# Performance work log

Hardware: AMD Instinct MI355X
Metric: run time of the kernel (lower is better)

Reference implementation:

```python
import jax, jax.numpy as jnp
import numpy as np

DIM = 768
N_HEADS = 12
HEAD_DIM = DIM // N_HEADS
SCALE = HEAD_DIM ** (-0.5)


def setup_inputs() -> dict:
    key = jax.random.key(0)
    k1, k2, k3 = jax.random.split(key, 3)
    B, S = 8, 1024
    x = jax.random.normal(k1, (B, S, DIM), dtype=jnp.float32)
    qkv_w = jax.random.normal(k2, (3 * DIM, DIM), dtype=jnp.float32) * (DIM ** -0.5)
    qkv_b = jnp.zeros((3 * DIM,), dtype=jnp.float32)
    proj_w = jax.random.normal(k3, (DIM, DIM), dtype=jnp.float32) * (DIM ** -0.5)
    proj_b = jnp.zeros((DIM,), dtype=jnp.float32)
    return {"x": x, "qkv_w": qkv_w, "qkv_b": qkv_b, "proj_w": proj_w, "proj_b": proj_b}


def reference(x, qkv_w, qkv_b, proj_w, proj_b):
    B, S, D = x.shape
    # qkv projection: (B,S,3D)
    qkv = jnp.einsum('bsd,ed->bse', x, qkv_w) + qkv_b
    qkv = qkv.reshape(B, S, 3, N_HEADS, HEAD_DIM)
    q, k, v = qkv[:, :, 0], qkv[:, :, 1], qkv[:, :, 2]  # each (B,S,H,Dh)
    # scaled dot-product attention, materializing (B,H,S,S) as the original does
    scores = jnp.einsum('bqhd,bkhd->bhqk', q, k) * SCALE
    attn = jax.nn.softmax(scores, axis=-1)
    out = jnp.einsum('bhqk,bkhd->bqhd', attn, v).reshape(B, S, D)
    # output projection
    return jnp.einsum('bsd,ed->bse', out, proj_w) + proj_b
```

## Files before the change

### kernel.cpp

```cpp
#include <hip/hip_runtime.h>
#include <hip/hip_bf16.h>


typedef __attribute__((ext_vector_type(4))) float  f32x4;
typedef __attribute__((ext_vector_type(8))) short  short8;
typedef __attribute__((ext_vector_type(4))) short  short4v;
typedef __attribute__((ext_vector_type(2))) unsigned int uint2v;

__device__ __forceinline__ unsigned short f2bf_hw(float f) {
  return __builtin_bit_cast(unsigned short, __float2bfloat16(f));
}
__device__ __forceinline__ unsigned int pk2bf(float a, float b) {
  return (unsigned int)f2bf_hw(a) | ((unsigned int)f2bf_hw(b) << 16);
}

#define MFMA16(a, b, c) __builtin_amdgcn_mfma_f32_16x16x32_bf16((a), (b), (c), 0, 0, 0)

#define QSCALE 0.18033688011112042f

__device__ __forceinline__ void gload_lds16(const unsigned short* g, char* lds) {
  __builtin_amdgcn_global_load_lds(
      (const __attribute__((address_space(1))) unsigned int*)g,
      (__attribute__((address_space(3))) unsigned int*)lds, 16, 0, 0);
}

__global__ __launch_bounds__(256)
void cvt3(const float* __restrict__ a, unsigned short* __restrict__ da, int na,
          const float* __restrict__ b, unsigned short* __restrict__ db, int nb,
          const float* __restrict__ c, unsigned short* __restrict__ dc)
{
  int i = blockIdx.x * 256 + threadIdx.x;
  const float* s; unsigned short* d;
  if (i < na)           { s = a; d = da; }
  else if (i < na + nb) { s = b; d = db; i -= na; }
  else                  { s = c; d = dc; i -= na + nb; }
  f32x4 v = ((const f32x4*)s)[i];
  short4v h;
  h[0] = (short)f2bf_hw(v[0]); h[1] = (short)f2bf_hw(v[1]);
  h[2] = (short)f2bf_hw(v[2]); h[3] = (short)f2bf_hw(v[3]);
  ((short4v*)d)[i] = h;
}

template<int EPI>
__global__ __launch_bounds__(256)
void gemm_bt(const unsigned short* __restrict__ A, const unsigned short* __restrict__ Wb,
             const float* __restrict__ bias,
             unsigned short* __restrict__ Qt, unsigned short* __restrict__ Kt,
             unsigned short* __restrict__ Vt, float* __restrict__ Out)
{
  __shared__ char lds[65536];
  const int tid = threadIdx.x;
  const int w = tid >> 6, l = tid & 63, lr = l & 15, lg = l >> 4;
  const int wr = w >> 1, wc = w & 1;
  const int m0 = blockIdx.x * 128, n0 = blockIdx.y * 128;
  f32x4 acc[4][4] = {};

  const int srow = tid >> 3;
  const int cb   = ((tid & 7) << 4) ^ ((srow & 7) << 4);
  const unsigned short* pA = A  + (size_t)(m0 + srow) * 768 + (cb >> 1);
  const unsigned short* pW = Wb + (size_t)(n0 + srow) * 768 + (cb >> 1);
  char* const ldsA = lds + tid * 16;
  char* const ldsW = lds + 16384 + tid * 16;

  #pragma unroll
  for (int c = 0; c < 4; ++c) gload_lds16(pA + c * 32 * 768, ldsA + c * 4096);
  #pragma unroll
  for (int c = 0; c < 4; ++c) gload_lds16(pW + c * 32 * 768, ldsW + c * 4096);
  pA += 64; pW += 64;

  for (int kt = 0; kt < 12; ++kt) {
    if (kt < 11) {
      const int nb = ((kt + 1) & 1) * 32768;
      #pragma unroll
      for (int c = 0; c < 4; ++c) gload_lds16(pA + c * 32 * 768, ldsA + nb + c * 4096);
      #pragma unroll
      for (int c = 0; c < 4; ++c) gload_lds16(pW + c * 32 * 768, ldsW + nb + c * 4096);
      pA += 64; pW += 64;
      asm volatile("s_waitcnt vmcnt(8)" ::: "memory");
    } else {
      asm volatile("s_waitcnt vmcnt(0)" ::: "memory");
    }
    __builtin_amdgcn_s_barrier();
    __builtin_amdgcn_sched_barrier(0);

    const char* Ab = lds + (kt & 1) * 32768;
    const char* Bb = Ab + 16384;
    #pragma unroll
    for (int kc = 0; kc < 2; ++kc) {
      short8 af[4], bfr[4];
      #pragma unroll
      for (int mf = 0; mf < 4; ++mf) {
        const int row = wr * 64 + mf * 16 + lr;
        af[mf] = *(const short8*)(Ab + row * 128 +
                                  ((kc * 64 + lg * 16) ^ ((row & 7) << 4)));
      }
      #pragma unroll
      for (int nf = 0; nf < 4; ++nf) {
        const int row = wc * 64 + nf * 16 + lr;
        bfr[nf] = *(const short8*)(Bb + row * 128 +
                                   ((kc * 64 + lg * 16) ^ ((row & 7) << 4)));
      }
      #pragma unroll
      for (int mf = 0; mf < 4; ++mf)
        #pragma unroll
        for (int nf = 0; nf < 4; ++nf)
          acc[mf][nf] = MFMA16(af[mf], bfr[nf], acc[mf][nf]);
    }
    __builtin_amdgcn_s_barrier();
  }

  if constexpr (EPI == 0) {
    const int tt = blockIdx.y / 6;
    const int h = (blockIdx.y % 6) * 2 + wc;
    #pragma unroll
    for (int nf = 0; nf < 4; ++nf) {
      const int dh = nf * 16 + lr;
      const float bv = bias[n0 + wc * 64 + dh];
      #pragma unroll
      for (int mf = 0; mf < 4; ++mf) {
        const int mb = m0 + wr * 64 + mf * 16 + lg * 4;
        const int b_ = mb >> 10, s_ = mb & 1023;
        f32x4 c = acc[mf][nf];
        if (tt == 0) {
          unsigned short* p = Qt + ((b_ * 12 + h) * 1024 + s_) * 64 + dh;
          #pragma unroll
          for (int j = 0; j < 4; ++j) p[j * 64] = f2bf_hw((c[j] + bv) * QSCALE);
        } else if (tt == 1) {
          unsigned short* p = Kt + ((b_ * 12 + h) * 1024 + s_) * 64 + dh;
          #pragma unroll
          for (int j = 0; j < 4; ++j) p[j * 64] = f2bf_hw(c[j] + bv);
        } else {
          short4v pk;
          #pragma unroll
          for (int j = 0; j < 4; ++j) pk[j] = (short)f2bf_hw(c[j] + bv);
          *(short4v*)(Vt + ((b_ * 12 + h) * 64 + dh) * 1024 + s_) = pk;
        }
      }
    }
  } else {
    #pragma unroll
    for (int nf = 0; nf < 4; ++nf) {
      const int e = n0 + wc * 64 + nf * 16 + lr;
      const float bv = bias[e];
      #pragma unroll
      for (int mf = 0; mf < 4; ++mf) {
        const int mb = m0 + wr * 64 + mf * 16 + lg * 4;
        #pragma unroll
        for (int j = 0; j < 4; ++j)
          Out[(size_t)(mb + j) * 768 + e] = acc[mf][nf][j] + bv;
      }
    }
  }
}

__global__ __launch_bounds__(256, 4)
void attn_fwd(const unsigned short* __restrict__ Qt,
              const unsigned short* __restrict__ Kt,
              const unsigned short* __restrict__ Vt,
              unsigned short* __restrict__ AO)
{
  __shared__ char lds[40960];
  char* Ks = lds;
  char* Vs = lds + 16384;
  char* Ps = lds + 32768;

  const int bid = blockIdx.x;
  const int bh = bid % 96, qt = bid / 96;
  const int tid = threadIdx.x, w = tid >> 6, l = tid & 63, lr = l & 15, lg = l >> 4;
  const unsigned short* Qh = Qt + bh * 65536;
  const unsigned short* Kh = Kt + bh * 65536;
  const unsigned short* Vh = Vt + bh * 65536;
  const int b_ = bh / 12, h = bh % 12;

  const int srow = tid >> 3;
  const int cb   = ((tid & 7) << 4) ^ ((srow & 7) << 4);
  char* const ldsK = Ks + tid * 16;
  char* const ldsV = Vs + tid * 16;
  char* const Pw = Ps + w * 2048;
  const int pswz = (lr & 7) << 4;

  #pragma unroll
  for (int c = 0; c < 2; ++c)
    gload_lds16(Kh + (size_t)(srow + c * 32) * 64 + (cb >> 1), ldsK + c * 4096);
  #pragma unroll
  for (int c = 0; c < 2; ++c)
    gload_lds16(Vh + (size_t)(srow + c * 32) * 1024 + (cb >> 1), ldsV + c * 4096);
  __syncthreads();

  for (int qs = 0; qs < 2; ++qs) {
    const int q0 = qt * 128 + qs * 64 + w * 16;
    const short8 aq0 = *(const short8*)(Qh + (q0 + lr) * 64 + lg * 8);
    const short8 aq1 = *(const short8*)(Qh + (q0 + lr) * 64 + 32 + lg * 8);

    float mr = -1e30f, lsum = 0.f;
    f32x4 o[4] = {};

    for (int t = 0; t < 16; ++t) {
      const int cur = t & 1;
      if (!(qs == 1 && t == 15)) {
        const int nk = ((t + 1) & 15) * 64;
        const int nb = (cur ^ 1) * 8192;
        #pragma unroll
        for (int c = 0; c < 2; ++c)
          gload_lds16(Kh + (size_t)(nk + srow + c * 32) * 64 + (cb >> 1),
                      ldsK + nb + c * 4096);
        #pragma unroll
        for (int c = 0; c < 2; ++c)
          gload_lds16(Vh + (size_t)(srow + c * 32) * 1024 + nk + (cb >> 1),
                      ldsV + nb + c * 4096);
      }

      const char* Kb = Ks + cur * 8192;
      f32x4 sf[4];
      __builtin_amdgcn_s_setprio(1);
      #pragma unroll
      for (int kf = 0; kf < 4; ++kf) {
        const char* base = Kb + (kf * 16 + lr) * 128;
        short8 b0 = *(const short8*)(base + ((lg * 16) ^ pswz));
        short8 b1 = *(const short8*)(base + ((64 + lg * 16) ^ pswz));
        f32x4 c = {};
        c = MFMA16(b0, aq0, c);
        c = MFMA16(b1, aq1, c);
        sf[kf] = c;
      }
      __builtin_amdgcn_s_setprio(0);

      float tm = fmaxf(fmaxf(sf[0][0], sf[0][1]), fmaxf(sf[0][2], sf[0][3]));
      #pragma unroll
      for (int kf = 1; kf < 4; ++kf)
        tm = fmaxf(tm, fmaxf(fmaxf(sf[kf][0], sf[kf][1]), fmaxf(sf[kf][2], sf[kf][3])));
      tm = fmaxf(tm, __shfl_xor(tm, 16));
      tm = fmaxf(tm, __shfl_xor(tm, 32));

      if (__any(tm > mr + 8.0f)) {
        const float mn = fmaxf(mr, tm);
        const float corr = exp2f(mr - mn);
        lsum *= corr;
        #pragma unroll
        for (int cf = 0; cf < 4; ++cf)
          #pragma unroll
          for (int j = 0; j < 4; ++j) o[cf][j] *= corr;
        mr = mn;
      }

      float ts = 0.f;
      #pragma unroll
      for (int kf = 0; kf < 4; ++kf) {
        const float p0 = exp2f(sf[kf][0] - mr);
        const float p1 = exp2f(sf[kf][1] - mr);
        const float p2 = exp2f(sf[kf][2] - mr);
        const float p3 = exp2f(sf[kf][3] - mr);
        ts += (p0 + p1) + (p2 + p3);
        uint2v pv; pv[0] = pk2bf(p0, p1); pv[1] = pk2bf(p2, p3);
        *(uint2v*)(Pw + lr * 128 + ((kf * 32 + lg * 8) ^ pswz)) = pv;
      }
      ts += __shfl_xor(ts, 16);
      ts += __shfl_xor(ts, 32);
      lsum += ts;

      asm volatile("s_waitcnt lgkmcnt(0)" ::: "memory");
      __builtin_amdgcn_sched_barrier(0);

      const char* Vb = Vs + cur * 8192;
      __builtin_amdgcn_s_setprio(1);
      #pragma unroll
      for (int kc = 0; kc < 2; ++kc) {
        short8 pa = *(const short8*)(Pw + lr * 128 + ((kc * 64 + lg * 16) ^ pswz));
        #pragma unroll
        for (int cf = 0; cf < 4; ++cf) {
          short8 bv = *(const short8*)(Vb + (cf * 16 + lr) * 128 +
                                       ((kc * 64 + lg * 16) ^ pswz));
          o[cf] = MFMA16(bv, pa, o[cf]);
        }
      }
      __builtin_amdgcn_s_setprio(0);

      __syncthreads();
    }

    const float inv = 1.f / lsum;
    unsigned short* aop = AO + ((size_t)(b_ * 1024 + q0 + lr)) * 768 + h * 64 + lg * 4;
    #pragma unroll
    for (int cf = 0; cf < 4; ++cf) {
      uint2v pv;
      pv[0] = pk2bf(o[cf][0] * inv, o[cf][1] * inv);
      pv[1] = pk2bf(o[cf][2] * inv, o[cf][3] * inv);
      *(uint2v*)(aop + cf * 16) = pv;
    }
  }
}

extern "C" void kernel_launch(void* const* d_in, const int* in_sizes, int n_in,
                              void* d_out, int out_size, void* d_ws, size_t ws_size,
                              hipStream_t stream)
{
  const float* x      = (const float*)d_in[0];
  const float* qkv_w  = (const float*)d_in[1];
  const float* qkv_b  = (const float*)d_in[2];
  const float* proj_w = (const float*)d_in[3];
  const float* proj_b = (const float*)d_in[4];
  float* out = (float*)d_out;

  unsigned short* ws = (unsigned short*)d_ws;
  unsigned short* xb  = ws;
  unsigned short* Qt  = ws + 6291456;
  unsigned short* Kt  = Qt + 6291456;
  unsigned short* Vt  = Kt + 6291456;
  unsigned short* qwb = Vt + 6291456;
  unsigned short* pwb = qwb + 1769472;
  unsigned short* AO  = xb;

  cvt3<<<8448, 256, 0, stream>>>(x, xb, 1572864, qkv_w, qwb, 442368, proj_w, pwb);
  gemm_bt<0><<<dim3(64, 18), 256, 0, stream>>>(xb, qwb, qkv_b, Qt, Kt, Vt, nullptr);
  attn_fwd<<<768, 256, 0, stream>>>(Qt, Kt, Vt, AO);
  gemm_bt<1><<<dim3(64, 6), 256, 0, stream>>>(AO, pwb, proj_b, nullptr, nullptr, nullptr, out);
}
```

Baseline: 125.4 us.

## Switch attention to 32x32x16 MFMA with register-resident P via lane shuffles

Rewrites the attention inner loop to use 32x32x16 bf16 MFMAs, with each wave owning 32 query rows for the full key sweep instead of two passes over 16-row chunks. The probability tile is no longer staged through LDS. It is packed to bf16 and rearranged between lane halves with xor-32 shuffles into the B-operand layout, which removes the P LDS buffer and its waitcnt. This is meant to cut LDS traffic, halve the K/V reload passes per block, and shrink shared memory. The cost is more accumulator registers (two 16-wide accumulators) and a longer serial softmax reduction over 16 values per lane.

```diff
diff --git a/kernel.cpp b/kernel.cpp
--- a/kernel.cpp
+++ b/kernel.cpp
@@ -2,10 +2,12 @@
 #include <hip/hip_bf16.h>
 
 
-typedef __attribute__((ext_vector_type(4))) float  f32x4;
-typedef __attribute__((ext_vector_type(8))) short  short8;
-typedef __attribute__((ext_vector_type(4))) short  short4v;
-typedef __attribute__((ext_vector_type(2))) unsigned int uint2v;
+typedef __attribute__((ext_vector_type(4)))  float f32x4;
+typedef __attribute__((ext_vector_type(16))) float f32x16;
+typedef __attribute__((ext_vector_type(8)))  short short8;
+typedef __attribute__((ext_vector_type(4)))  short short4v;
+typedef __attribute__((ext_vector_type(2)))  unsigned int uint2v;
+typedef __attribute__((ext_vector_type(4)))  unsigned int uint4v;
 
 __device__ __forceinline__ unsigned short f2bf_hw(float f) {
   return __builtin_bit_cast(unsigned short, __float2bfloat16(f));
@@ -15,6 +17,7 @@
 }
 
 #define MFMA16(a, b, c) __builtin_amdgcn_mfma_f32_16x16x32_bf16((a), (b), (c), 0, 0, 0)
+#define MFMA32(a, b, c) __builtin_amdgcn_mfma_f32_32x32x16_bf16((a), (b), (c), 0, 0, 0)
 
 #define QSCALE 0.18033688011112042f
 
@@ -159,14 +162,14 @@
               const unsigned short* __restrict__ Vt,
               unsigned short* __restrict__ AO)
 {
-  __shared__ char lds[40960];
+  __shared__ char lds[32768];
   char* Ks = lds;
   char* Vs = lds + 16384;
-  char* Ps = lds + 32768;
 
   const int bid = blockIdx.x;
   const int bh = bid % 96, qt = bid / 96;
-  const int tid = threadIdx.x, w = tid >> 6, l = tid & 63, lr = l & 15, lg = l >> 4;
+  const int tid = threadIdx.x, w = tid >> 6, l = tid & 63;
+  const int l31 = l & 31, hi = l >> 5;
   const unsigned short* Qh = Qt + bh * 65536;
   const unsigned short* Kh = Kt + bh * 65536;
   const unsigned short* Vh = Vt + bh * 65536;
@@ -176,8 +179,12 @@
   const int cb   = ((tid & 7) << 4) ^ ((srow & 7) << 4);
   char* const ldsK = Ks + tid * 16;
   char* const ldsV = Vs + tid * 16;
-  char* const Pw = Ps + w * 2048;
-  const int pswz = (lr & 7) << 4;
+
+  const int q0 = qt * 128 + w * 32;
+  const unsigned short* qp = Qh + (size_t)(q0 + l31) * 64 + hi * 8;
+  short8 bq[4];
+  #pragma unroll
+  for (int kk = 0; kk < 4; ++kk) bq[kk] = *(const short8*)(qp + kk * 16);
 
   #pragma unroll
   for (int c = 0; c < 2; ++c)
@@ -187,49 +194,44 @@
     gload_lds16(Vh + (size_t)(srow + c * 32) * 1024 + (cb >> 1), ldsV + c * 4096);
   __syncthreads();
 
-  for (int qs = 0; qs < 2; ++qs) {
-    const int q0 = qt * 128 + qs * 64 + w * 16;
-    const short8 aq0 = *(const short8*)(Qh + (q0 + lr) * 64 + lg * 8);
-    const short8 aq1 = *(const short8*)(Qh + (q0 + lr) * 64 + 32 + lg * 8);
-
-    float mr = -1e30f, lsum = 0.f;
-    f32x4 o[4] = {};
-
-    for (int t = 0; t < 16; ++t) {
-      const int cur = t & 1;
-      if (!(qs == 1 && t == 15)) {
-        const int nk = ((t + 1) & 15) * 64;
-        const int nb = (cur ^ 1) * 8192;
-        #pragma unroll
-        for (int c = 0; c < 2; ++c)
-          gload_lds16(Kh + (size_t)(nk + srow + c * 32) * 64 + (cb >> 1),
-                      ldsK + nb + c * 4096);
-        #pragma unroll
-        for (int c = 0; c < 2; ++c)
-          gload_lds16(Vh + (size_t)(srow + c * 32) * 1024 + nk + (cb >> 1),
-                      ldsV + nb + c * 4096);
-      }
-
-      const char* Kb = Ks + cur * 8192;
-      f32x4 sf[4];
+  float mr = -1e30f, lsum = 0.f;
+  f32x16 o0 = {}, o1 = {};
+
+  for (int t = 0; t < 16; ++t) {
+    const int cur = t & 1;
+    if (t < 15) {
+      const int nk = (t + 1) * 64;
+      const int nb = (cur ^ 1) * 8192;
+      #pragma unroll
+      for (int c = 0; c < 2; ++c)
+        gload_lds16(Kh + (size_t)(nk + srow + c * 32) * 64 + (cb >> 1),
+                    ldsK + nb + c * 4096);
+      #pragma unroll
+      for (int c = 0; c < 2; ++c)
+        gload_lds16(Vh + (size_t)(srow + c * 32) * 1024 + nk + (cb >> 1),
+                    ldsV + nb + c * 4096);
+    }
+
+    const char* Kb = Ks + cur * 8192;
+    const char* Vb = Vs + cur * 8192;
+
+    #pragma unroll
+    for (int kb = 0; kb < 2; ++kb) {
+      const int krow = kb * 32 + l31;
+      const char* kbase = Kb + krow * 128;
+      const int kswz = (krow & 7) << 4;
+      f32x16 s = {};
       __builtin_amdgcn_s_setprio(1);
       #pragma unroll
-      for (int kf = 0; kf < 4; ++kf) {
-        const char* base = Kb + (kf * 16 + lr) * 128;
-        short8 b0 = *(const short8*)(base + ((lg * 16) ^ pswz));
-        short8 b1 = *(const short8*)(base + ((64 + lg * 16) ^ pswz));
-        f32x4 c = {};
-        c = MFMA16(b0, aq0, c);
-        c = MFMA16(b1, aq1, c);
-        sf[kf] = c;
+      for (int kk = 0; kk < 4; ++kk) {
+        short8 ka = *(const short8*)(kbase + ((kk * 32 + hi * 16) ^ kswz));
+        s = MFMA32(ka, bq[kk], s);
       }
       __builtin_amdgcn_s_setprio(0);
 
-      float tm = fmaxf(fmaxf(sf[0][0], sf[0][1]), fmaxf(sf[0][2], sf[0][3]));
-      #pragma unroll
-      for (int kf = 1; kf < 4; ++kf)
-        tm = fmaxf(tm, fmaxf(fmaxf(sf[kf][0], sf[kf][1]), fmaxf(sf[kf][2], sf[kf][3])));
-      tm = fmaxf(tm, __shfl_xor(tm, 16));
+      float tm = s[0];
+      #pragma unroll
+      for (int i = 1; i < 16; ++i) tm = fmaxf(tm, s[i]);
       tm = fmaxf(tm, __shfl_xor(tm, 32));
 
       if (__any(tm > mr + 8.0f)) {
@@ -237,56 +239,62 @@
         const float corr = exp2f(mr - mn);
         lsum *= corr;
         #pragma unroll
-        for (int cf = 0; cf < 4; ++cf)
-          #pragma unroll
-          for (int j = 0; j < 4; ++j) o[cf][j] *= corr;
+        for (int i = 0; i < 16; ++i) { o0[i] *= corr; o1[i] *= corr; }
         mr = mn;
       }
 
       float ts = 0.f;
-      #pragma unroll
-      for (int kf = 0; kf < 4; ++kf) {
-        const float p0 = exp2f(sf[kf][0] - mr);
-        const float p1 = exp2f(sf[kf][1] - mr);
-        const float p2 = exp2f(sf[kf][2] - mr);
-        const float p3 = exp2f(sf[kf][3] - mr);
-        ts += (p0 + p1) + (p2 + p3);
-        uint2v pv; pv[0] = pk2bf(p0, p1); pv[1] = pk2bf(p2, p3);
-        *(uint2v*)(Pw + lr * 128 + ((kf * 32 + lg * 8) ^ pswz)) = pv;
-      }
-      ts += __shfl_xor(ts, 16);
+      unsigned int pk_[8];
+      #pragma unroll
+      for (int i = 0; i < 8; ++i) {
+        const float pa = exp2f(s[2 * i]     - mr);
+        const float pb = exp2f(s[2 * i + 1] - mr);
+        ts += pa + pb;
+        pk_[i] = pk2bf(pa, pb);
+      }
       ts += __shfl_xor(ts, 32);
       lsum += ts;
 
-      asm volatile("s_waitcnt lgkmcnt(0)" ::: "memory");
-      __builtin_amdgcn_sched_barrier(0);
-
-      const char* Vb = Vs + cur * 8192;
+      const unsigned int x0 = __shfl_xor(pk_[0], 32), x1 = __shfl_xor(pk_[1], 32);
+      const unsigned int x2 = __shfl_xor(pk_[2], 32), x3 = __shfl_xor(pk_[3], 32);
+      const unsigned int x4 = __shfl_xor(pk_[4], 32), x5 = __shfl_xor(pk_[5], 32);
+      const unsigned int x6 = __shfl_xor(pk_[6], 32), x7 = __shfl_xor(pk_[7], 32);
+      uint4v b0v, b1v;
+      b0v[0] = hi ? x2 : pk_[0];  b0v[1] = hi ? x3 : pk_[1];
+      b0v[2] = hi ? pk_[2] : x0;  b0v[3] = hi ? pk_[3] : x1;
+      b1v[0] = hi ? x6 : pk_[4];  b1v[1] = hi ? x7 : pk_[5];
+      b1v[2] = hi ? pk_[6] : x4;  b1v[3] = hi ? pk_[7] : x5;
+      const short8 pb0 = __builtin_bit_cast(short8, b0v);
+      const short8 pb1 = __builtin_bit_cast(short8, b1v);
+
+      const int vswz = (l31 & 7) << 4;
       __builtin_amdgcn_s_setprio(1);
       #pragma unroll
-      for (int kc = 0; kc < 2; ++kc) {
-        short8 pa = *(const short8*)(Pw + lr * 128 + ((kc * 64 + lg * 16) ^ pswz));
-        #pragma unroll
-        for (int cf = 0; cf < 4; ++cf) {
-          short8 bv = *(const short8*)(Vb + (cf * 16 + lr) * 128 +
-                                       ((kc * 64 + lg * 16) ^ pswz));
-          o[cf] = MFMA16(bv, pa, o[cf]);
-        }
+      for (int kk = 0; kk < 2; ++kk) {
+        const short8 pbk = kk ? pb1 : pb0;
+        const int koff = kb * 64 + kk * 32 + hi * 16;
+        short8 va0 = *(const short8*)(Vb + l31 * 128 + (koff ^ vswz));
+        o0 = MFMA32(va0, pbk, o0);
+        short8 va1 = *(const short8*)(Vb + (32 + l31) * 128 + (koff ^ vswz));
+        o1 = MFMA32(va1, pbk, o1);
       }
       __builtin_amdgcn_s_setprio(0);
-
-      __syncthreads();
-    }
-
-    const float inv = 1.f / lsum;
-    unsigned short* aop = AO + ((size_t)(b_ * 1024 + q0 + lr)) * 768 + h * 64 + lg * 4;
-    #pragma unroll
-    for (int cf = 0; cf < 4; ++cf) {
-      uint2v pv;
-      pv[0] = pk2bf(o[cf][0] * inv, o[cf][1] * inv);
-      pv[1] = pk2bf(o[cf][2] * inv, o[cf][3] * inv);
-      *(uint2v*)(aop + cf * 16) = pv;
-    }
+    }
+
+    __syncthreads();
+  }
+
+  const float inv = 1.f / lsum;
+  unsigned short* aop = AO + ((size_t)(b_ * 1024 + q0 + l31)) * 768 + h * 64;
+  #pragma unroll
+  for (int g = 0; g < 4; ++g) {
+    uint2v s0, s1;
+    s0[0] = pk2bf(o0[4 * g] * inv,     o0[4 * g + 1] * inv);
+    s0[1] = pk2bf(o0[4 * g + 2] * inv, o0[4 * g + 3] * inv);
+    *(uint2v*)(aop + g * 8 + 4 * hi) = s0;
+    s1[0] = pk2bf(o1[4 * g] * inv,     o1[4 * g + 1] * inv);
+    s1[1] = pk2bf(o1[4 * g + 2] * inv, o1[4 * g + 3] * inv);
+    *(uint2v*)(aop + 32 + g * 8 + 4 * hi) = s1;
   }
 }
 
```

New measurement: 118.9 us. -5.2%, faster.
